# Kernel optimization log

Hardware: AMD Instinct MI355X
Metric: run time of the kernel (lower is better)

## Reference

```python
import jax, jax.numpy as jnp
import numpy as np

B, N, D = 2, 8192, 64          # batch, points, feature dim (dim_in == dim_out)
FILTER_SIZE = 11               # k nearest neighbors in feature space
N_ITER = 5                     # mean-field iterations


def setup_inputs() -> dict:
    key = jax.random.key(0)
    k0, k1, k2, k3 = jax.random.split(key, 4)
    return {
        "logits": jax.random.normal(k0, (B, N), jnp.float32),
        "p": jax.random.normal(k1, (B, D, N), jnp.float32),
        "W1": jax.random.normal(k2, (D, D), jnp.float32) / np.float32(np.sqrt(D)),
        "b1": jnp.zeros((D,), jnp.float32),
        "W2": jax.random.normal(k3, (D, D), jnp.float32) / np.float32(np.sqrt(D)),
        "b2": jnp.zeros((D,), jnp.float32),
    }


def reference(logits, p, W1, b1, W2, b2):
    # crf_encoder: two stacked Linear layers applied to p.permute(0,2,1) -> [B,N,D]
    f = jnp.einsum('bdn,de->bne', p, W1) + b1
    f = jnp.einsum('bne,ef->bnf', f, W2) + b2  # [B,N,D] feature embedding

    # pairwise squared distances in feature space: [B,N,N]
    sq = jnp.sum(f * f, axis=-1)
    d2 = sq[:, :, None] + sq[:, None, :] - 2.0 * jnp.einsum('bnd,bmd->bnm', f, f)

    # filter_size nearest neighbors (includes self) with Gaussian weights exp(-d2)
    neg_d2, idx = jax.lax.top_k(-d2, FILTER_SIZE)   # [B,N,K]
    w = jnp.exp(neg_d2)                             # [B,N,K]

    gather = jax.vmap(lambda qb, ib: qb[ib])        # per-batch gather: [N],[N,K]->[N,K]

    # mean-field iterations (binary CRF: sigmoid marginals, unary = logits)
    u = logits
    for _ in range(N_ITER):
        q = jax.nn.sigmoid(u)                       # current marginals [B,N]
        msg = jnp.sum(w * gather(q, idx), axis=-1)  # filtered message   [B,N]
        u = logits - msg                            # compatibility transform + unary

    return jax.nn.sigmoid(u)  # return_log_proba=False -> probabilities, [B,N]
```

## Files before the change

### kernel.cpp

```cpp
#include <hip/hip_runtime.h>

#define NPTS 8192
#define NTOT 16384
#define KNB 11
#define CAP 16
#define MARG 9.0f

typedef __attribute__((ext_vector_type(8))) short short8;
typedef __attribute__((ext_vector_type(4))) float f32x4;

__device__ __forceinline__ unsigned short f2bf(float x) {
  union { float f; unsigned u; } v; v.f = x;
  unsigned r = v.u + 0x7FFFu + ((v.u >> 16) & 1u);
  return (unsigned short)(r >> 16);
}

__device__ __forceinline__ float sigm(float x) { return 1.f / (1.f + expf(-x)); }

__global__ __launch_bounds__(256) void k0_w12(
    const float* __restrict__ W1, const float* __restrict__ b1,
    const float* __restrict__ W2, const float* __restrict__ b2,
    float* __restrict__ W12, float* __restrict__ b12,
    unsigned* __restrict__ cnt,
    const float* __restrict__ logits, float* __restrict__ q0) {
  int t = blockIdx.x * 256 + threadIdx.x;
  cnt[t] = 0u;
  q0[t] = sigm(logits[t]);
  if (t >= 4096) return;
  int d = t >> 6, e = t & 63;
  float s = 0.f;
  for (int kk = 0; kk < 64; ++kk) s = fmaf(W1[d * 64 + kk], W2[kk * 64 + e], s);
  W12[t] = s;
  if (d == 0) {
    float sb = b2[e];
    for (int kk = 0; kk < 64; ++kk) sb = fmaf(b1[kk], W2[kk * 64 + e], sb);
    b12[e] = sb;
  }
}

__global__ __launch_bounds__(256) void k1_encode(
    const float* __restrict__ p,
    const float* __restrict__ W12,
    const float* __restrict__ b12,
    float* __restrict__ f32f,
    unsigned short* __restrict__ fpre,
    float* __restrict__ sq,
    float* __restrict__ sq32) {
  __shared__ float sPart[4][64];
  int t = threadIdx.x, lane = t & 63;
  int w = __builtin_amdgcn_readfirstlane(t >> 6);
  int e0 = w * 16;
  int base = blockIdx.x * 64;
  int b = base >> 13, n0 = base & (NPTS - 1);
  const float* pb = p + (size_t)b * 64 * NPTS + n0 + lane;

  float f[16];
#pragma unroll
  for (int j = 0; j < 16; ++j) f[j] = b12[e0 + j];

#pragma unroll 8
  for (int d = 0; d < 64; ++d) {
    float pd = pb[(size_t)d * NPTS];
#pragma unroll
    for (int j = 0; j < 16; ++j)
      f[j] = fmaf(pd, W12[d * 64 + e0 + j], f[j]);
  }

  float s = 0.f;
#pragma unroll
  for (int j = 0; j < 16; ++j) s = fmaf(f[j], f[j], s);
  sPart[w][lane] = s;
  __syncthreads();
  if (w == 0) {
    float s32 = sPart[0][lane] + sPart[1][lane];
    float s64 = s32 + (sPart[2][lane] + sPart[3][lane]);
    sq32[base + lane] = s32;
    sq[base + lane] = s64;
  }

  f32x4* o4 = (f32x4*)(f32f + (size_t)(base + lane) * 64 + e0);
#pragma unroll
  for (int jj = 0; jj < 4; ++jj) {
    f32x4 v; v[0] = f[4 * jj]; v[1] = f[4 * jj + 1]; v[2] = f[4 * jj + 2]; v[3] = f[4 * jj + 3];
    o4[jj] = v;
  }
  if (w < 2) {
    unsigned* ob = (unsigned*)(fpre + (size_t)(base + lane) * 32 + e0);
#pragma unroll
    for (int jj = 0; jj < 8; ++jj) {
      unsigned lo = f2bf(f[2 * jj]);
      unsigned hi = f2bf(f[2 * jj + 1]);
      ob[jj] = lo | (hi << 16);
    }
  }
}

__global__ __launch_bounds__(256) void k2_gram_select(
    const unsigned short* __restrict__ fpre,
    const float* __restrict__ sq32,
    unsigned* __restrict__ cnt,
    unsigned* __restrict__ cand) {
  __shared__ uint4 sB[1024];
  int bid = blockIdx.x;
  int b = (bid >= 528) ? 1 : 0;
  int rem = bid - b * 528;
  int band = (int)((sqrtf(8.f * (float)rem + 1.f) - 1.f) * 0.5f);
  if (((band + 1) * (band + 2)) / 2 <= rem) band++;
  else if ((band * (band + 1)) / 2 > rem) band--;
  int seg = rem - (band * (band + 1)) / 2;

  int t = threadIdx.x;
  int lane = t & 63;
  int arow = lane & 15;
  int q = lane >> 4;
  int wave = t >> 6;
  int rowbase = band * 256 + wave * 64;
  int cbase = seg * 256;
  const unsigned short* fb = fpre + (size_t)b * NPTS * 32;
  const float* s32b = sq32 + b * NPTS;

  const uint4* gsrc = (const uint4*)fb + (size_t)seg * 1024;
  uint4 v[4];
#pragma unroll
  for (int k = 0; k < 4; ++k) v[k] = gsrc[t + k * 256];

  short8 afrag[4];
#pragma unroll
  for (int tr = 0; tr < 4; ++tr)
    afrag[tr] = *(const short8*)(fb + (size_t)(rowbase + tr * 16 + arow) * 32 + q * 8);

  f32x4 srq[4], hh[4];
#pragma unroll
  for (int tr = 0; tr < 4; ++tr) {
    srq[tr] = *(const f32x4*)(s32b + rowbase + tr * 16 + (q << 2));
    hh[tr] = 0.5f * srq[tr];
  }
  float thrc[16];
#pragma unroll
  for (int cc = 0; cc < 4; ++cc)
#pragma unroll
    for (int tc = 0; tc < 4; ++tc)
      thrc[cc * 4 + tc] = 0.5f * s32b[cbase + cc * 64 + tc * 16 + arow] - 0.5f * MARG;

#pragma unroll
  for (int k = 0; k < 4; ++k) {
    int c = t + k * 256;
    int r = c >> 2, qq = c & 3;
    sB[r * 4 + (qq ^ (r & 3))] = v[k];
  }
  __syncthreads();

  f32x4 z4 = {0.f, 0.f, 0.f, 0.f};
  unsigned hitmask = 0u;
#pragma unroll
  for (int cc = 0; cc < 4; ++cc)
#pragma unroll
    for (int tc = 0; tc < 4; ++tc) {
      int e = cc * 4 + tc;
      int rl = cc * 64 + tc * 16 + arow;
      short8 bf = *(const short8*)&sB[rl * 4 + (q ^ (rl & 3))];
      f32x4 a0 = __builtin_amdgcn_mfma_f32_16x16x32_bf16(afrag[0], bf, z4, 0, 0, 0);
      f32x4 a1 = __builtin_amdgcn_mfma_f32_16x16x32_bf16(afrag[1], bf, z4, 0, 0, 0);
      f32x4 a2 = __builtin_amdgcn_mfma_f32_16x16x32_bf16(afrag[2], bf, z4, 0, 0, 0);
      f32x4 a3 = __builtin_amdgcn_mfma_f32_16x16x32_bf16(afrag[3], bf, z4, 0, 0, 0);
      float m0 = fmaxf(fmaxf(a0[0] - hh[0][0], a0[1] - hh[0][1]),
                       fmaxf(a0[2] - hh[0][2], a0[3] - hh[0][3]));
      float m1 = fmaxf(fmaxf(a1[0] - hh[1][0], a1[1] - hh[1][1]),
                       fmaxf(a1[2] - hh[1][2], a1[3] - hh[1][3]));
      float m2 = fmaxf(fmaxf(a2[0] - hh[2][0], a2[1] - hh[2][1]),
                       fmaxf(a2[2] - hh[2][2], a2[3] - hh[2][3]));
      float m3 = fmaxf(fmaxf(a3[0] - hh[3][0], a3[1] - hh[3][1]),
                       fmaxf(a3[2] - hh[3][2], a3[3] - hh[3][3]));
      float m = fmaxf(fmaxf(m0, m1), fmaxf(m2, m3));
      if (__ballot(m > thrc[e])) hitmask |= (1u << e);
    }

  if (hitmask) {
#pragma unroll 1
    for (int e = 0; e < 16; ++e) {
      if (!(hitmask & (1u << e))) continue;
      int cc = e >> 2, tc = e & 3;
      int rl = cc * 64 + tc * 16 + arow;
      short8 bf = *(const short8*)&sB[rl * 4 + (q ^ (rl & 3))];
      int colpt = cbase + cc * 64 + tc * 16 + arow;
      float scv = s32b[colpt];
      f32x4 acc[4];
#pragma unroll
      for (int tr = 0; tr < 4; ++tr)
        acc[tr] = __builtin_amdgcn_mfma_f32_16x16x32_bf16(afrag[tr], bf, z4, 0, 0, 0);
#pragma unroll
      for (int tr = 0; tr < 4; ++tr)
#pragma unroll
        for (int rg = 0; rg < 4; ++rg) {
          float d2 = srq[tr][rg] + scv - 2.f * acc[tr][rg];
          if (d2 < MARG) {
            int rowpt = rowbase + tr * 16 + (q << 2) + rg;
            int gr = b * NPTS + rowpt;
            union { float f; unsigned u; } cv; cv.f = d2 + 16.f;
            unsigned kb = cv.u & 0xFFFFE000u;
            unsigned slot = atomicAdd(&cnt[gr], 1u);
            if (slot < CAP) cand[gr * CAP + slot] = kb | (unsigned)colpt;
            if (band != seg) {
              int gc = b * NPTS + colpt;
              unsigned slot2 = atomicAdd(&cnt[gc], 1u);
              if (slot2 < CAP) cand[gc * CAP + slot2] = kb | (unsigned)rowpt;
            }
          }
        }
    }
  }
}

__global__ __launch_bounds__(256) void k3_refine(
    const float* __restrict__ f32f, const float* __restrict__ sq,
    const unsigned* __restrict__ cnt, const unsigned* __restrict__ cand,
    float* __restrict__ W, int* __restrict__ IDX) {
  int r = blockIdx.x * 256 + threadIdx.x;
  int b = r >> 13;
  unsigned count = cnt[r];
  if (count > CAP) count = CAP;
  if (count <= 1) return;

  unsigned k[CAP];
#pragma unroll
  for (int j = 0; j < CAP; ++j)
    k[j] = (j < (int)count) ? cand[r * CAP + j] : 0xFFFFFFFFu;
#pragma unroll
  for (int a = 0; a < CAP - 1; ++a)
#pragma unroll
    for (int c = 0; c < CAP - 1; ++c) {
      unsigned lo = min(k[c], k[c + 1]);
      unsigned hi = max(k[c], k[c + 1]);
      k[c] = lo; k[c + 1] = hi;
    }

  float fr[64];
  const f32x4* fr4 = (const f32x4*)(f32f + (size_t)r * 64);
#pragma unroll
  for (int j = 0; j < 16; ++j) {
    f32x4 v = fr4[j];
    fr[4 * j] = v[0]; fr[4 * j + 1] = v[1]; fr[4 * j + 2] = v[2]; fr[4 * j + 3] = v[3];
  }
  float sqr = sq[r];
  int nsel = (int)count < KNB ? (int)count : KNB;
#pragma unroll
  for (int kk = 0; kk < KNB; ++kk) {
    float w = 0.f;
    int gi = r;
    if (kk < nsel) {
      int col = (int)(k[kk] & 8191u);
      gi = b * NPTS + col;
      const float* fm = f32f + (size_t)gi * 64;
      float dot = 0.f;
#pragma unroll
      for (int d = 0; d < 64; ++d) dot = fmaf(fr[d], fm[d], dot);
      float d2 = sqr + sq[gi] - 2.f * dot;
      w = expf(-d2);
    }
    W[r * KNB + kk] = w;
    IDX[r * KNB + kk] = gi;
  }
}

__global__ __launch_bounds__(256) void k4_iter(
    const float* __restrict__ logits, const unsigned* __restrict__ cnt,
    const float* __restrict__ W, const int* __restrict__ IDX,
    const float* __restrict__ qin, float* __restrict__ qout,
    float* __restrict__ out) {
  int i = blockIdx.x * 256 + threadIdx.x;
  unsigned c = cnt[i];
  float msg;
  if (c <= 1u) {
    msg = qin[i];
  } else {
    msg = 0.f;
    const float* wp = W + (size_t)i * KNB;
    const int* ip = IDX + (size_t)i * KNB;
#pragma unroll
    for (int kk = 0; kk < KNB; ++kk) msg = fmaf(wp[kk], qin[ip[kk]], msg);
  }
  float u = logits[i] - msg;
  float qv = sigm(u);
  qout[i] = qv;
  out[i] = qv;
}

extern "C" void kernel_launch(void* const* d_in, const int* in_sizes, int n_in,
                              void* d_out, int out_size, void* d_ws, size_t ws_size,
                              hipStream_t stream) {
  const float* logits = (const float*)d_in[0];
  const float* p      = (const float*)d_in[1];
  const float* W1     = (const float*)d_in[2];
  const float* b1     = (const float*)d_in[3];
  const float* W2     = (const float*)d_in[4];
  const float* b2     = (const float*)d_in[5];
  float* out = (float*)d_out;

  char* ws = (char*)d_ws;
  float* W12 = (float*)ws;
  float* b12 = W12 + 4096;
  float* f32f = b12 + 64;
  unsigned short* fpre = (unsigned short*)(f32f + (size_t)NTOT * 64);
  float* sq = (float*)(fpre + (size_t)NTOT * 32);
  float* sq32 = sq + NTOT;
  unsigned* cnt = (unsigned*)(sq32 + NTOT);
  unsigned* cand = cnt + NTOT;
  float* Wbuf = (float*)(cand + (size_t)NTOT * CAP);
  int* IDX = (int*)(Wbuf + (size_t)NTOT * KNB);
  float* qA = (float*)(IDX + (size_t)NTOT * KNB);
  float* qB = qA + NTOT;

  k0_w12<<<64, 256, 0, stream>>>(W1, b1, W2, b2, W12, b12, cnt, logits, qA);
  k1_encode<<<256, 256, 0, stream>>>(p, W12, b12, f32f, fpre, sq, sq32);
  k2_gram_select<<<1056, 256, 0, stream>>>(fpre, sq32, cnt, cand);
  k3_refine<<<64, 256, 0, stream>>>(f32f, sq, cnt, cand, Wbuf, IDX);
  k4_iter<<<64, 256, 0, stream>>>(logits, cnt, Wbuf, IDX, qA, qB, out);
  k4_iter<<<64, 256, 0, stream>>>(logits, cnt, Wbuf, IDX, qB, qA, out);
  k4_iter<<<64, 256, 0, stream>>>(logits, cnt, Wbuf, IDX, qA, qB, out);
  k4_iter<<<64, 256, 0, stream>>>(logits, cnt, Wbuf, IDX, qB, qA, out);
  k4_iter<<<64, 256, 0, stream>>>(logits, cnt, Wbuf, IDX, qA, qB, out);
}
```

Before: 120.1 us.

## Fuse neighbor refine and mean-field iterations into one per-batch kernel

```diff
diff --git a/kernel.cpp b/kernel.cpp
--- a/kernel.cpp
+++ b/kernel.cpp
@@ -21,11 +21,9 @@
     const float* __restrict__ W1, const float* __restrict__ b1,
     const float* __restrict__ W2, const float* __restrict__ b2,
     float* __restrict__ W12, float* __restrict__ b12,
-    unsigned* __restrict__ cnt,
-    const float* __restrict__ logits, float* __restrict__ q0) {
+    unsigned* __restrict__ cnt) {
   int t = blockIdx.x * 256 + threadIdx.x;
   cnt[t] = 0u;
-  q0[t] = sigm(logits[t]);
   if (t >= 4096) return;
   int d = t >> 6, e = t & 63;
   float s = 0.f;
@@ -46,13 +44,23 @@
     unsigned short* __restrict__ fpre,
     float* __restrict__ sq,
     float* __restrict__ sq32) {
+  __shared__ float sp[64 * 64];
   __shared__ float sPart[4][64];
   int t = threadIdx.x, lane = t & 63;
   int w = __builtin_amdgcn_readfirstlane(t >> 6);
   int e0 = w * 16;
   int base = blockIdx.x * 64;
   int b = base >> 13, n0 = base & (NPTS - 1);
-  const float* pb = p + (size_t)b * 64 * NPTS + n0 + lane;
+  const float* pb = p + (size_t)b * 64 * NPTS + n0;
+
+  int row = t >> 4, chunk = t & 15;
+#pragma unroll
+  for (int k = 0; k < 4; ++k) {
+    int r = k * 16 + row;
+    uint4 v = *(const uint4*)(pb + (size_t)r * NPTS + chunk * 4);
+    *(uint4*)(sp + r * 64 + chunk * 4) = v;
+  }
+  __syncthreads();
 
   float f[16];
 #pragma unroll
@@ -60,7 +68,7 @@
 
 #pragma unroll 8
   for (int d = 0; d < 64; ++d) {
-    float pd = pb[(size_t)d * NPTS];
+    float pd = sp[d * 64 + lane];
 #pragma unroll
     for (int j = 0; j < 16; ++j)
       f[j] = fmaf(pd, W12[d * 64 + e0 + j], f[j]);
@@ -211,78 +219,95 @@
   }
 }
 
-__global__ __launch_bounds__(256) void k3_refine(
+__global__ __launch_bounds__(1024) void k_tail(
     const float* __restrict__ f32f, const float* __restrict__ sq,
     const unsigned* __restrict__ cnt, const unsigned* __restrict__ cand,
-    float* __restrict__ W, int* __restrict__ IDX) {
-  int r = blockIdx.x * 256 + threadIdx.x;
-  int b = r >> 13;
-  unsigned count = cnt[r];
-  if (count > CAP) count = CAP;
-  if (count <= 1) return;
-
-  unsigned k[CAP];
-#pragma unroll
-  for (int j = 0; j < CAP; ++j)
-    k[j] = (j < (int)count) ? cand[r * CAP + j] : 0xFFFFFFFFu;
-#pragma unroll
-  for (int a = 0; a < CAP - 1; ++a)
-#pragma unroll
-    for (int c = 0; c < CAP - 1; ++c) {
-      unsigned lo = min(k[c], k[c + 1]);
-      unsigned hi = max(k[c], k[c + 1]);
-      k[c] = lo; k[c + 1] = hi;
-    }
-
-  float fr[64];
-  const f32x4* fr4 = (const f32x4*)(f32f + (size_t)r * 64);
-#pragma unroll
-  for (int j = 0; j < 16; ++j) {
-    f32x4 v = fr4[j];
-    fr[4 * j] = v[0]; fr[4 * j + 1] = v[1]; fr[4 * j + 2] = v[2]; fr[4 * j + 3] = v[3];
-  }
-  float sqr = sq[r];
-  int nsel = (int)count < KNB ? (int)count : KNB;
-#pragma unroll
-  for (int kk = 0; kk < KNB; ++kk) {
-    float w = 0.f;
-    int gi = r;
-    if (kk < nsel) {
-      int col = (int)(k[kk] & 8191u);
-      gi = b * NPTS + col;
-      const float* fm = f32f + (size_t)gi * 64;
-      float dot = 0.f;
-#pragma unroll
-      for (int d = 0; d < 64; ++d) dot = fmaf(fr[d], fm[d], dot);
-      float d2 = sqr + sq[gi] - 2.f * dot;
-      w = expf(-d2);
-    }
-    W[r * KNB + kk] = w;
-    IDX[r * KNB + kk] = gi;
-  }
-}
-
-__global__ __launch_bounds__(256) void k4_iter(
-    const float* __restrict__ logits, const unsigned* __restrict__ cnt,
-    const float* __restrict__ W, const int* __restrict__ IDX,
-    const float* __restrict__ qin, float* __restrict__ qout,
-    float* __restrict__ out) {
-  int i = blockIdx.x * 256 + threadIdx.x;
-  unsigned c = cnt[i];
-  float msg;
-  if (c <= 1u) {
-    msg = qin[i];
-  } else {
-    msg = 0.f;
-    const float* wp = W + (size_t)i * KNB;
-    const int* ip = IDX + (size_t)i * KNB;
-#pragma unroll
-    for (int kk = 0; kk < KNB; ++kk) msg = fmaf(wp[kk], qin[ip[kk]], msg);
-  }
-  float u = logits[i] - msg;
-  float qv = sigm(u);
-  qout[i] = qv;
-  out[i] = qv;
+    float* __restrict__ Wbuf, int* __restrict__ IDXb,
+    const float* __restrict__ logits, float* __restrict__ out) {
+  __shared__ float qs[NPTS];
+  int t = threadIdx.x;
+  int rb = blockIdx.x * NPTS;
+  int bb = blockIdx.x;
+  float lg[8];
+  unsigned c[8];
+
+#pragma unroll 1
+  for (int j = 0; j < 8; ++j) {
+    int il = j * 1024 + t;
+    int r = rb + il;
+    lg[j] = logits[r];
+    qs[il] = sigm(lg[j]);
+    unsigned count = cnt[r];
+    c[j] = count;
+    if (count > CAP) count = CAP;
+    if (count > 1) {
+      unsigned k[CAP];
+#pragma unroll
+      for (int jj = 0; jj < CAP; ++jj)
+        k[jj] = (jj < (int)count) ? cand[r * CAP + jj] : 0xFFFFFFFFu;
+#pragma unroll
+      for (int a = 0; a < CAP - 1; ++a)
+#pragma unroll
+        for (int cc = 0; cc < CAP - 1; ++cc) {
+          unsigned lo = min(k[cc], k[cc + 1]);
+          unsigned hi = max(k[cc], k[cc + 1]);
+          k[cc] = lo; k[cc + 1] = hi;
+        }
+      float fr[64];
+      const f32x4* fr4 = (const f32x4*)(f32f + (size_t)r * 64);
+#pragma unroll
+      for (int jj = 0; jj < 16; ++jj) {
+        f32x4 v = fr4[jj];
+        fr[4 * jj] = v[0]; fr[4 * jj + 1] = v[1]; fr[4 * jj + 2] = v[2]; fr[4 * jj + 3] = v[3];
+      }
+      float sqr = sq[r];
+      int nsel = (int)count < KNB ? (int)count : KNB;
+#pragma unroll 1
+      for (int kk = 0; kk < KNB; ++kk) {
+        float w = 0.f;
+        int gi = r;
+        if (kk < nsel) {
+          int col = (int)(k[kk] & 8191u);
+          gi = bb * NPTS + col;
+          const float* fm = f32f + (size_t)gi * 64;
+          float dot = 0.f;
+#pragma unroll
+          for (int d = 0; d < 64; ++d) dot = fmaf(fr[d], fm[d], dot);
+          float d2 = sqr + sq[gi] - 2.f * dot;
+          w = expf(-d2);
+        }
+        Wbuf[(size_t)r * KNB + kk] = w;
+        IDXb[(size_t)r * KNB + kk] = gi;
+      }
+    }
+  }
+  __threadfence();
+  __syncthreads();
+
+  float u[8];
+  for (int it = 0; it < 5; ++it) {
+#pragma unroll
+    for (int j = 0; j < 8; ++j) {
+      int il = j * 1024 + t;
+      float msg;
+      if (c[j] <= 1u) {
+        msg = qs[il];
+      } else {
+        msg = 0.f;
+        const float* wp = Wbuf + (size_t)(rb + il) * KNB;
+        const int* ip = IDXb + (size_t)(rb + il) * KNB;
+#pragma unroll
+        for (int kk = 0; kk < KNB; ++kk) msg = fmaf(wp[kk], qs[ip[kk] - rb], msg);
+      }
+      u[j] = lg[j] - msg;
+    }
+    __syncthreads();
+#pragma unroll
+    for (int j = 0; j < 8; ++j) qs[j * 1024 + t] = sigm(u[j]);
+    __syncthreads();
+  }
+#pragma unroll
+  for (int j = 0; j < 8; ++j) out[rb + j * 1024 + t] = sigm(u[j]);
 }
 
 extern "C" void kernel_launch(void* const* d_in, const int* in_sizes, int n_in,
@@ -307,16 +332,9 @@
   unsigned* cand = cnt + NTOT;
   float* Wbuf = (float*)(cand + (size_t)NTOT * CAP);
   int* IDX = (int*)(Wbuf + (size_t)NTOT * KNB);
-  float* qA = (float*)(IDX + (size_t)NTOT * KNB);
-  float* qB = qA + NTOT;
-
-  k0_w12<<<64, 256, 0, stream>>>(W1, b1, W2, b2, W12, b12, cnt, logits, qA);
+
+  k0_w12<<<64, 256, 0, stream>>>(W1, b1, W2, b2, W12, b12, cnt);
   k1_encode<<<256, 256, 0, stream>>>(p, W12, b12, f32f, fpre, sq, sq32);
   k2_gram_select<<<1056, 256, 0, stream>>>(fpre, sq32, cnt, cand);
-  k3_refine<<<64, 256, 0, stream>>>(f32f, sq, cnt, cand, Wbuf, IDX);
-  k4_iter<<<64, 256, 0, stream>>>(logits, cnt, Wbuf, IDX, qA, qB, out);
-  k4_iter<<<64, 256, 0, stream>>>(logits, cnt, Wbuf, IDX, qB, qA, out);
-  k4_iter<<<64, 256, 0, stream>>>(logits, cnt, Wbuf, IDX, qA, qB, out);
-  k4_iter<<<64, 256, 0, stream>>>(logits, cnt, Wbuf, IDX, qB, qA, out);
-  k4_iter<<<64, 256, 0, stream>>>(logits, cnt, Wbuf, IDX, qA, qB, out);
-}
+  k_tail<<<2, 1024, 0, stream>>>(f32f, sq, cnt, cand, Wbuf, IDX, logits, out);
+}
```

New measurement: 144.8 us. +20.5%, slower.
